# Performance work log

Hardware: AMD Instinct MI355X
Metric: run time of the kernel (lower is better)

## Reference

```python
import jax, jax.numpy as jnp
import numpy as np

N_NODES = 200_000
N_EDGES = 400_000
EMB_DIM = 128
HID_DIM = 24
N_TYPES = 8


def setup_inputs() -> dict:
    key = jax.random.key(0)
    k_emb, k_src, k_typ, k_w1, k_w2 = jax.random.split(key, 5)
    rgcn_emb = jax.random.normal(k_emb, (N_NODES, EMB_DIM), dtype=jnp.float32)
    edge_index = jax.random.randint(k_src, (2, N_EDGES), 0, N_NODES, dtype=jnp.int32)
    edge_type = jax.random.randint(k_typ, (N_EDGES,), 0, N_TYPES, dtype=jnp.int32)
    # per-edge-type 2-layer MLP params: Linear(2D->H), Linear(H->1)
    W1 = jax.random.normal(k_w1, (N_TYPES, 2 * EMB_DIM, HID_DIM), dtype=jnp.float32) * 0.05
    b1 = jnp.zeros((N_TYPES, HID_DIM), dtype=jnp.float32)
    W2 = jax.random.normal(k_w2, (N_TYPES, HID_DIM), dtype=jnp.float32) * 0.05
    b2 = jnp.zeros((N_TYPES,), dtype=jnp.float32)
    return {"rgcn_emb": rgcn_emb, "edge_index": edge_index, "edge_type": edge_type,
            "W1": W1, "b1": b1, "W2": W2, "b2": b2}


def reference(rgcn_emb, edge_index, edge_type, W1, b1, W2, b2):
    src, dst = edge_index[0], edge_index[1]
    # gather + concat: [E, 2D]
    edge_emb = jnp.concatenate([rgcn_emb[src], rgcn_emb[dst]], axis=-1)
    # dense per-type expert compute, then select by routing (MoE-style)
    h = jnp.einsum('ed,tdh->teh', edge_emb, W1) + b1[:, None, :]  # [T,E,H]
    h = jnp.where(h > 0, h, 0.01 * h)  # LeakyReLU(0.01)
    s = jnp.einsum('teh,th->te', h, W2) + b2[:, None]  # [T,E]
    onehot = jax.nn.one_hot(edge_type, N_TYPES, dtype=s.dtype)  # [E,T]
    scores = jnp.einsum('te,et->e', s, onehot)  # scatter-select per edge
    return (scores, rgcn_emb)
```

## Files before the change

kernel.cpp:

```cpp
#include <hip/hip_runtime.h>


typedef _Float16 h2 __attribute__((ext_vector_type(2)));

constexpr int N_NODES = 200000;
constexpr int N_EDGES = 400000;
constexpr int EMB_DIM = 128;
constexpr int HID     = 24;
constexpr int N_TYPES = 8;
constexpr int BLK     = 256;

constexpr int MAX_PAD      = N_EDGES + N_TYPES * (BLK - 1);
constexpr int SCORE_BLOCKS = (MAX_PAD + BLK - 1) / BLK;
constexpr int COPY_BLOCKS  = 1024;
constexpr int HIST_BLOCKS  = 128;
constexpr int SC_BLOCKS    = 128;
constexpr int SC_CH        = (N_EDGES + SC_BLOCKS - 1) / SC_BLOCKS;
constexpr int CV_BLOCKS    = 1536;

constexpr size_t SORT_BYTES = (size_t)(16 + MAX_PAD) * sizeof(int);
constexpr size_t EMB16_OFF  = (SORT_BYTES + 255) & ~(size_t)255;
constexpr size_t EMB16_BYTES = (size_t)N_NODES * EMB_DIM * 2;
constexpr size_t W16_OFF    = EMB16_OFF + EMB16_BYTES;
constexpr size_t W16_BYTES  = (size_t)N_TYPES * 128 * HID * 4;
constexpr size_t NEED16     = W16_OFF + W16_BYTES;

__device__ __forceinline__ float fdot2f(h2 a, h2 b, float c) {
#if __has_builtin(__builtin_amdgcn_fdot2)
    return __builtin_amdgcn_fdot2(a, b, c, false);
#else
    return c + (float)a[0] * (float)b[0] + (float)a[1] * (float)b[1];
#endif
}

__global__ __launch_bounds__(BLK) void hist_k(const int* __restrict__ etype,
                                              int* __restrict__ counts) {
    __shared__ int lc[N_TYPES];
    if (threadIdx.x < N_TYPES) lc[threadIdx.x] = 0;
    __syncthreads();
    for (int e = blockIdx.x * BLK + threadIdx.x; e < N_EDGES; e += HIST_BLOCKS * BLK)
        atomicAdd(&lc[etype[e]], 1);
    __syncthreads();
    if (threadIdx.x < N_TYPES) {
        int v = lc[threadIdx.x];
        if (v) atomicAdd(&counts[threadIdx.x], v);
    }
}

__global__ __launch_bounds__(BLK) void scatter_convert_k(
        const int* __restrict__ etype, int* __restrict__ counts,
        int* __restrict__ sorted,
        const float* __restrict__ emb, h2* __restrict__ emb16,
        const float* __restrict__ W1, h2* __restrict__ w16, int do16) {
    int b = blockIdx.x;
    if (b < SC_BLOCKS) {
        __shared__ int lc[N_TYPES], base[N_TYPES];
        if (threadIdx.x < N_TYPES) lc[threadIdx.x] = 0;
        __syncthreads();
        int e0 = b * SC_CH, e1 = min(e0 + SC_CH, N_EDGES);
        for (int e = e0 + threadIdx.x; e < e1; e += BLK)
            atomicAdd(&lc[etype[e]], 1);
        __syncthreads();
        if (threadIdx.x < N_TYPES)
            base[threadIdx.x] = atomicAdd(&counts[8 + threadIdx.x], lc[threadIdx.x]);
        __syncthreads();
        if (threadIdx.x < N_TYPES) lc[threadIdx.x] = 0;
        __syncthreads();
        int poff[N_TYPES];
        int off = 0;
#pragma unroll
        for (int t = 0; t < N_TYPES; ++t) {
            poff[t] = off;
            off += ((counts[t] + BLK - 1) / BLK) * BLK;
        }
        for (int e = e0 + threadIdx.x; e < e1; e += BLK) {
            int t = etype[e];
            int r = atomicAdd(&lc[t], 1);
            sorted[poff[t] + base[t] + r] = e;
        }
    } else if (do16) {
        int cb = b - SC_BLOCKS;
        if (cb < 16) {
            for (int p = cb * BLK + threadIdx.x; p < N_TYPES * 128 * HID; p += 16 * BLK) {
                int t   = p / (128 * HID);
                int rem = p - t * 128 * HID;
                int kp  = rem / HID, j = rem - kp * HID;
                h2 v;
                v[0] = (_Float16)W1[(t * 256 + 2 * kp)     * HID + j];
                v[1] = (_Float16)W1[(t * 256 + 2 * kp + 1) * HID + j];
                w16[p] = v;
            }
        }
        const float4* in4 = (const float4*)emb;
        int4* o16 = (int4*)emb16;
        const int ngrp = N_NODES * EMB_DIM / 8;
        for (int g = cb * BLK + threadIdx.x; g < ngrp; g += CV_BLOCKS * BLK) {
            float4 a = in4[2 * g], c = in4[2 * g + 1];
            union { int4 v; h2 h[4]; } u;
            u.h[0] = h2{(_Float16)a.x, (_Float16)a.y};
            u.h[1] = h2{(_Float16)a.z, (_Float16)a.w};
            u.h[2] = h2{(_Float16)c.x, (_Float16)c.y};
            u.h[3] = h2{(_Float16)c.z, (_Float16)c.w};
            o16[g] = u.v;
        }
    }
}

__device__ __forceinline__ void do_copy(const float* __restrict__ emb,
                                        float* __restrict__ out, int cb, int nb) {
    const float4* s4 = (const float4*)emb;
    float4* o4 = (float4*)(out + N_EDGES);
    const long long n4 = (long long)N_NODES * EMB_DIM / 4;
    long long stride = (long long)nb * BLK;
    for (long long i = (long long)cb * BLK + threadIdx.x; i < n4; i += stride)
        o4[i] = s4[i];
}

__global__ __launch_bounds__(BLK) void score16_k(
        const unsigned short* __restrict__ emb16u, const float* __restrict__ emb,
        const int* __restrict__ srci, const int* __restrict__ dsti,
        const int* __restrict__ counts, const int* __restrict__ sorted,
        const h2* __restrict__ w16, const float* __restrict__ b1,
        const float* __restrict__ W2, const float* __restrict__ b2,
        float* __restrict__ out) {
    int b = blockIdx.x;
    if (b >= SCORE_BLOCKS) {
        do_copy(emb, out, b - SCORE_BLOCKS, (int)gridDim.x - SCORE_BLOCKS);
        return;
    }
    int poff[N_TYPES];
    int off = 0;
#pragma unroll
    for (int t = 0; t < N_TYPES; ++t) {
        poff[t] = off;
        off += ((counts[t] + BLK - 1) / BLK) * BLK;
    }
    int slot0 = b * BLK;
    if (slot0 >= off) return;
    int t = 0;
#pragma unroll
    for (int i = 1; i < N_TYPES; ++i)
        if (slot0 >= poff[i]) t = i;
    t = __builtin_amdgcn_readfirstlane(t);
    int cnt = counts[t];
    int local = slot0 - poff[t] + (int)threadIdx.x;
    if (local >= cnt) return;
    int e = sorted[slot0 + threadIdx.x];
    int s = srci[e], d = dsti[e];

    float acc[HID];
#pragma unroll
    for (int j = 0; j < HID; ++j) acc[j] = b1[t * HID + j];
    const h2* wt = w16 + (size_t)t * 128 * HID;
    const int4* x0 = (const int4*)(emb16u + (size_t)s * EMB_DIM);
    const int4* x1 = (const int4*)(emb16u + (size_t)d * EMB_DIM);

#pragma unroll 1
    for (int half = 0; half < 2; ++half) {
        const int4* xp = half ? x1 : x0;
#pragma unroll 1
        for (int c = 0; c < 2; ++c) {
            int4 r[8];
#pragma unroll
            for (int k = 0; k < 8; ++k) r[k] = xp[c * 8 + k];
            const h2* hp = (const h2*)r;
            const h2* wrow = wt + (half * 64 + c * 32) * HID;
#pragma unroll
            for (int kp = 0; kp < 32; ++kp) {
#pragma unroll
                for (int j = 0; j < HID; ++j)
                    acc[j] = fdot2f(hp[kp], wrow[kp * HID + j], acc[j]);
            }
        }
    }
    float sc = b2[t];
#pragma unroll
    for (int j = 0; j < HID; ++j) {
        float h = acc[j];
        h = (h > 0.f) ? h : 0.01f * h;
        sc = fmaf(h, W2[t * HID + j], sc);
    }
    out[e] = sc;
}

__device__ __forceinline__ void half_mm(const float4* __restrict__ x4,
                                        const float* __restrict__ w,
                                        float acc[HID]) {
#pragma unroll 1
    for (int c = 0; c < 4; ++c) {
        float4 r[8];
#pragma unroll
        for (int k = 0; k < 8; ++k) r[k] = x4[c * 8 + k];
#pragma unroll
        for (int k = 0; k < 8; ++k) {
            const float* wp = w + (c * 32 + k * 4) * HID;
#pragma unroll
            for (int j = 0; j < HID; ++j) acc[j] = fmaf(r[k].x, wp[0 * HID + j], acc[j]);
#pragma unroll
            for (int j = 0; j < HID; ++j) acc[j] = fmaf(r[k].y, wp[1 * HID + j], acc[j]);
#pragma unroll
            for (int j = 0; j < HID; ++j) acc[j] = fmaf(r[k].z, wp[2 * HID + j], acc[j]);
#pragma unroll
            for (int j = 0; j < HID; ++j) acc[j] = fmaf(r[k].w, wp[3 * HID + j], acc[j]);
        }
    }
}

__global__ __launch_bounds__(BLK) void score32_k(
        const float* __restrict__ emb,
        const int* __restrict__ srci, const int* __restrict__ dsti,
        const int* __restrict__ counts, const int* __restrict__ sorted,
        const float* __restrict__ W1, const float* __restrict__ b1,
        const float* __restrict__ W2, const float* __restrict__ b2,
        float* __restrict__ out) {
    int b = blockIdx.x;
    if (b >= SCORE_BLOCKS) {
        do_copy(emb, out, b - SCORE_BLOCKS, (int)gridDim.x - SCORE_BLOCKS);
        return;
    }
    int poff[N_TYPES];
    int off = 0;
#pragma unroll
    for (int t = 0; t < N_TYPES; ++t) {
        poff[t] = off;
        off += ((counts[t] + BLK - 1) / BLK) * BLK;
    }
    int slot0 = b * BLK;
    if (slot0 >= off) return;
    int t = 0;
#pragma unroll
    for (int i = 1; i < N_TYPES; ++i)
        if (slot0 >= poff[i]) t = i;
    t = __builtin_amdgcn_readfirstlane(t);
    int cnt = counts[t];
    int local = slot0 - poff[t] + (int)threadIdx.x;
    if (local >= cnt) return;
    int e = sorted[slot0 + threadIdx.x];
    float acc[HID];
#pragma unroll
    for (int j = 0; j < HID; ++j) acc[j] = b1[t * HID + j];
    const float* W1t = W1 + (size_t)t * (2 * EMB_DIM * HID);
    int s = srci[e], d = dsti[e];
    half_mm((const float4*)(emb + (size_t)s * EMB_DIM), W1t, acc);
    half_mm((const float4*)(emb + (size_t)d * EMB_DIM), W1t + EMB_DIM * HID, acc);
    float sc = b2[t];
#pragma unroll
    for (int j = 0; j < HID; ++j) {
        float h = acc[j];
        h = (h > 0.f) ? h : 0.01f * h;
        sc = fmaf(h, W2[t * HID + j], sc);
    }
    out[e] = sc;
}

extern "C" void kernel_launch(void* const* d_in, const int* in_sizes, int n_in,
                              void* d_out, int out_size, void* d_ws, size_t ws_size,
                              hipStream_t stream) {
    const float* emb   = (const float*)d_in[0];
    const int*   eidx  = (const int*)d_in[1];
    const int*   etype = (const int*)d_in[2];
    const float* W1    = (const float*)d_in[3];
    const float* b1    = (const float*)d_in[4];
    const float* W2    = (const float*)d_in[5];
    const float* b2    = (const float*)d_in[6];
    float* out = (float*)d_out;
    const int* srci = eidx;
    const int* dsti = eidx + N_EDGES;

    if (ws_size >= SORT_BYTES) {
        int* counts = (int*)d_ws;
        int* sorted = counts + 16;
        bool f16 = (ws_size >= NEED16);
        h2* emb16 = (h2*)((char*)d_ws + EMB16_OFF);
        h2* w16   = (h2*)((char*)d_ws + W16_OFF);
        hipMemsetAsync(counts, 0, 16 * sizeof(int), stream);
        hist_k<<<HIST_BLOCKS, BLK, 0, stream>>>(etype, counts);
        scatter_convert_k<<<SC_BLOCKS + (f16 ? CV_BLOCKS : 0), BLK, 0, stream>>>(
            etype, counts, sorted, emb, emb16, W1, w16, f16 ? 1 : 0);
        if (f16) {
            score16_k<<<SCORE_BLOCKS + COPY_BLOCKS, BLK, 0, stream>>>(
                (const unsigned short*)emb16, emb, srci, dsti, counts, sorted,
                w16, b1, W2, b2, out);
        } else {
            score32_k<<<SCORE_BLOCKS + COPY_BLOCKS, BLK, 0, stream>>>(
                emb, srci, dsti, counts, sorted, W1, b1, W2, b2, out);
        }
    } else {
        score32_k<<<SCORE_BLOCKS + COPY_BLOCKS, BLK, 0, stream>>>(
            emb, srci, dsti, nullptr, nullptr, W1, b1, W2, b2, out);
    }
}
```

Baseline: 278.1 us.

## Fuse embedding copy into fp16 conversion pass and double-buffer row loads

The pass-through copy of rgcn_emb to the output moves into the prep kernel, so each fp32 element is read once, with nontemporal loads and stores, and both copied and converted to fp16. The histogram folds into the same prep launch using int4 loads of edge types, and the scatter becomes its own kernel. The score kernel no longer carries copy blocks and issues the next 128-byte chunk load before computing the current one, to overlap gather latency with the dot products. The fallback path becomes a simple unsorted fp32 kernel.

```diff
diff --git a/kernel.cpp b/kernel.cpp
--- a/kernel.cpp
+++ b/kernel.cpp
@@ -2,6 +2,7 @@
 
 
 typedef _Float16 h2 __attribute__((ext_vector_type(2)));
+typedef float    f4 __attribute__((ext_vector_type(4)));
 
 constexpr int N_NODES = 200000;
 constexpr int N_EDGES = 400000;
@@ -12,18 +13,20 @@
 
 constexpr int MAX_PAD      = N_EDGES + N_TYPES * (BLK - 1);
 constexpr int SCORE_BLOCKS = (MAX_PAD + BLK - 1) / BLK;
-constexpr int COPY_BLOCKS  = 1024;
-constexpr int HIST_BLOCKS  = 128;
 constexpr int SC_BLOCKS    = 128;
 constexpr int SC_CH        = (N_EDGES + SC_BLOCKS - 1) / SC_BLOCKS;
-constexpr int CV_BLOCKS    = 1536;
-
-constexpr size_t SORT_BYTES = (size_t)(16 + MAX_PAD) * sizeof(int);
-constexpr size_t EMB16_OFF  = (SORT_BYTES + 255) & ~(size_t)255;
+
+constexpr int PREP_HIST   = 64;
+constexpr int PREP_W1     = 16;
+constexpr int PREP_CONV   = 1968;
+constexpr int PREP_BLOCKS = PREP_HIST + PREP_W1 + PREP_CONV;
+
+constexpr size_t SORT_BYTES  = (size_t)(16 + MAX_PAD) * sizeof(int);
+constexpr size_t EMB16_OFF   = (SORT_BYTES + 255) & ~(size_t)255;
 constexpr size_t EMB16_BYTES = (size_t)N_NODES * EMB_DIM * 2;
-constexpr size_t W16_OFF    = EMB16_OFF + EMB16_BYTES;
-constexpr size_t W16_BYTES  = (size_t)N_TYPES * 128 * HID * 4;
-constexpr size_t NEED16     = W16_OFF + W16_BYTES;
+constexpr size_t W16_OFF     = EMB16_OFF + EMB16_BYTES;
+constexpr size_t W16_BYTES   = (size_t)N_TYPES * 128 * HID * 4;
+constexpr size_t NEED16      = W16_OFF + W16_BYTES;
 
 __device__ __forceinline__ float fdot2f(h2 a, h2 b, float c) {
 #if __has_builtin(__builtin_amdgcn_fdot2)
@@ -33,101 +36,103 @@
 #endif
 }
 
-__global__ __launch_bounds__(BLK) void hist_k(const int* __restrict__ etype,
-                                              int* __restrict__ counts) {
-    __shared__ int lc[N_TYPES];
-    if (threadIdx.x < N_TYPES) lc[threadIdx.x] = 0;
-    __syncthreads();
-    for (int e = blockIdx.x * BLK + threadIdx.x; e < N_EDGES; e += HIST_BLOCKS * BLK)
-        atomicAdd(&lc[etype[e]], 1);
-    __syncthreads();
-    if (threadIdx.x < N_TYPES) {
-        int v = lc[threadIdx.x];
-        if (v) atomicAdd(&counts[threadIdx.x], v);
-    }
-}
-
-__global__ __launch_bounds__(BLK) void scatter_convert_k(
+__global__ __launch_bounds__(BLK) void prep_k(
         const int* __restrict__ etype, int* __restrict__ counts,
-        int* __restrict__ sorted,
-        const float* __restrict__ emb, h2* __restrict__ emb16,
-        const float* __restrict__ W1, h2* __restrict__ w16, int do16) {
+        const float* __restrict__ emb, float* __restrict__ out,
+        int2* __restrict__ emb16, const float* __restrict__ W1,
+        h2* __restrict__ w16) {
     int b = blockIdx.x;
-    if (b < SC_BLOCKS) {
-        __shared__ int lc[N_TYPES], base[N_TYPES];
+    if (b < PREP_HIST) {
+        __shared__ int lc[N_TYPES];
         if (threadIdx.x < N_TYPES) lc[threadIdx.x] = 0;
         __syncthreads();
-        int e0 = b * SC_CH, e1 = min(e0 + SC_CH, N_EDGES);
-        for (int e = e0 + threadIdx.x; e < e1; e += BLK)
-            atomicAdd(&lc[etype[e]], 1);
+        const int4* et4 = (const int4*)etype;
+        for (int g = b * BLK + threadIdx.x; g < N_EDGES / 4; g += PREP_HIST * BLK) {
+            int4 v = et4[g];
+            atomicAdd(&lc[v.x], 1); atomicAdd(&lc[v.y], 1);
+            atomicAdd(&lc[v.z], 1); atomicAdd(&lc[v.w], 1);
+        }
         __syncthreads();
-        if (threadIdx.x < N_TYPES)
-            base[threadIdx.x] = atomicAdd(&counts[8 + threadIdx.x], lc[threadIdx.x]);
-        __syncthreads();
-        if (threadIdx.x < N_TYPES) lc[threadIdx.x] = 0;
-        __syncthreads();
-        int poff[N_TYPES];
-        int off = 0;
-#pragma unroll
-        for (int t = 0; t < N_TYPES; ++t) {
-            poff[t] = off;
-            off += ((counts[t] + BLK - 1) / BLK) * BLK;
-        }
-        for (int e = e0 + threadIdx.x; e < e1; e += BLK) {
-            int t = etype[e];
-            int r = atomicAdd(&lc[t], 1);
-            sorted[poff[t] + base[t] + r] = e;
-        }
-    } else if (do16) {
-        int cb = b - SC_BLOCKS;
-        if (cb < 16) {
-            for (int p = cb * BLK + threadIdx.x; p < N_TYPES * 128 * HID; p += 16 * BLK) {
-                int t   = p / (128 * HID);
-                int rem = p - t * 128 * HID;
-                int kp  = rem / HID, j = rem - kp * HID;
-                h2 v;
-                v[0] = (_Float16)W1[(t * 256 + 2 * kp)     * HID + j];
-                v[1] = (_Float16)W1[(t * 256 + 2 * kp + 1) * HID + j];
-                w16[p] = v;
-            }
-        }
-        const float4* in4 = (const float4*)emb;
-        int4* o16 = (int4*)emb16;
-        const int ngrp = N_NODES * EMB_DIM / 8;
-        for (int g = cb * BLK + threadIdx.x; g < ngrp; g += CV_BLOCKS * BLK) {
-            float4 a = in4[2 * g], c = in4[2 * g + 1];
-            union { int4 v; h2 h[4]; } u;
+        if (threadIdx.x < N_TYPES) {
+            int v = lc[threadIdx.x];
+            if (v) atomicAdd(&counts[threadIdx.x], v);
+        }
+    } else if (b < PREP_HIST + PREP_W1) {
+        int cb = b - PREP_HIST;
+        for (int p = cb * BLK + threadIdx.x; p < N_TYPES * 128 * HID; p += PREP_W1 * BLK) {
+            int t   = p / (128 * HID);
+            int rem = p - t * 128 * HID;
+            int kp  = rem / HID, j = rem - kp * HID;
+            h2 v;
+            v[0] = (_Float16)W1[(t * 256 + 2 * kp)     * HID + j];
+            v[1] = (_Float16)W1[(t * 256 + 2 * kp + 1) * HID + j];
+            w16[p] = v;
+        }
+    } else {
+        int cb = b - PREP_HIST - PREP_W1;
+        const f4* in4 = (const f4*)emb;
+        f4* o4 = (f4*)(out + N_EDGES);
+        const int n4 = N_NODES * EMB_DIM / 4;
+        for (int i = cb * BLK + threadIdx.x; i < n4; i += PREP_CONV * BLK) {
+            f4 a = __builtin_nontemporal_load(&in4[i]);
+            __builtin_nontemporal_store(a, &o4[i]);
+            union { int2 v; h2 h[2]; } u;
             u.h[0] = h2{(_Float16)a.x, (_Float16)a.y};
             u.h[1] = h2{(_Float16)a.z, (_Float16)a.w};
-            u.h[2] = h2{(_Float16)c.x, (_Float16)c.y};
-            u.h[3] = h2{(_Float16)c.z, (_Float16)c.w};
-            o16[g] = u.v;
-        }
-    }
-}
-
-__device__ __forceinline__ void do_copy(const float* __restrict__ emb,
-                                        float* __restrict__ out, int cb, int nb) {
-    const float4* s4 = (const float4*)emb;
-    float4* o4 = (float4*)(out + N_EDGES);
-    const long long n4 = (long long)N_NODES * EMB_DIM / 4;
-    long long stride = (long long)nb * BLK;
-    for (long long i = (long long)cb * BLK + threadIdx.x; i < n4; i += stride)
-        o4[i] = s4[i];
-}
-
-__global__ __launch_bounds__(BLK) void score16_k(
-        const unsigned short* __restrict__ emb16u, const float* __restrict__ emb,
+            emb16[i] = u.v;
+        }
+    }
+}
+
+__global__ __launch_bounds__(BLK) void scatter_k(
+        const int* __restrict__ etype, int* __restrict__ counts,
+        int* __restrict__ sorted) {
+    __shared__ int lc[N_TYPES], base[N_TYPES];
+    int b = blockIdx.x;
+    if (threadIdx.x < N_TYPES) lc[threadIdx.x] = 0;
+    __syncthreads();
+    int e0 = b * SC_CH, e1 = min(e0 + SC_CH, N_EDGES);
+    for (int e = e0 + threadIdx.x; e < e1; e += BLK)
+        atomicAdd(&lc[etype[e]], 1);
+    __syncthreads();
+    if (threadIdx.x < N_TYPES)
+        base[threadIdx.x] = atomicAdd(&counts[8 + threadIdx.x], lc[threadIdx.x]);
+    __syncthreads();
+    if (threadIdx.x < N_TYPES) lc[threadIdx.x] = 0;
+    __syncthreads();
+    int poff[N_TYPES];
+    int off = 0;
+#pragma unroll
+    for (int t = 0; t < N_TYPES; ++t) {
+        poff[t] = off;
+        off += ((counts[t] + BLK - 1) / BLK) * BLK;
+    }
+    for (int e = e0 + threadIdx.x; e < e1; e += BLK) {
+        int t = etype[e];
+        int r = atomicAdd(&lc[t], 1);
+        sorted[poff[t] + base[t] + r] = e;
+    }
+}
+
+__device__ __forceinline__ void compute_chunk(const int4* __restrict__ r,
+                                              const h2* __restrict__ wrow,
+                                              float acc[HID]) {
+    const h2* hp = (const h2*)r;
+#pragma unroll
+    for (int kp = 0; kp < 32; ++kp) {
+#pragma unroll
+        for (int j = 0; j < HID; ++j)
+            acc[j] = fdot2f(hp[kp], wrow[kp * HID + j], acc[j]);
+    }
+}
+
+__global__ __launch_bounds__(BLK) void score16_ns_k(
+        const unsigned short* __restrict__ emb16u,
         const int* __restrict__ srci, const int* __restrict__ dsti,
         const int* __restrict__ counts, const int* __restrict__ sorted,
         const h2* __restrict__ w16, const float* __restrict__ b1,
         const float* __restrict__ W2, const float* __restrict__ b2,
         float* __restrict__ out) {
-    int b = blockIdx.x;
-    if (b >= SCORE_BLOCKS) {
-        do_copy(emb, out, b - SCORE_BLOCKS, (int)gridDim.x - SCORE_BLOCKS);
-        return;
-    }
     int poff[N_TYPES];
     int off = 0;
 #pragma unroll
@@ -135,7 +140,7 @@
         poff[t] = off;
         off += ((counts[t] + BLK - 1) / BLK) * BLK;
     }
-    int slot0 = b * BLK;
+    int slot0 = blockIdx.x * BLK;
     if (slot0 >= off) return;
     int t = 0;
 #pragma unroll
@@ -155,24 +160,20 @@
     const int4* x0 = (const int4*)(emb16u + (size_t)s * EMB_DIM);
     const int4* x1 = (const int4*)(emb16u + (size_t)d * EMB_DIM);
 
-#pragma unroll 1
-    for (int half = 0; half < 2; ++half) {
-        const int4* xp = half ? x1 : x0;
-#pragma unroll 1
-        for (int c = 0; c < 2; ++c) {
-            int4 r[8];
-#pragma unroll
-            for (int k = 0; k < 8; ++k) r[k] = xp[c * 8 + k];
-            const h2* hp = (const h2*)r;
-            const h2* wrow = wt + (half * 64 + c * 32) * HID;
-#pragma unroll
-            for (int kp = 0; kp < 32; ++kp) {
-#pragma unroll
-                for (int j = 0; j < HID; ++j)
-                    acc[j] = fdot2f(hp[kp], wrow[kp * HID + j], acc[j]);
-            }
-        }
-    }
+    int4 A[8], B[8];
+#pragma unroll
+    for (int k = 0; k < 8; ++k) A[k] = x0[k];
+#pragma unroll
+    for (int k = 0; k < 8; ++k) B[k] = x0[8 + k];
+    compute_chunk(A, wt + 0 * 32 * HID, acc);
+#pragma unroll
+    for (int k = 0; k < 8; ++k) A[k] = x1[k];
+    compute_chunk(B, wt + 1 * 32 * HID, acc);
+#pragma unroll
+    for (int k = 0; k < 8; ++k) B[k] = x1[8 + k];
+    compute_chunk(A, wt + 2 * 32 * HID, acc);
+    compute_chunk(B, wt + 3 * 32 * HID, acc);
+
     float sc = b2[t];
 #pragma unroll
     for (int j = 0; j < HID; ++j) {
@@ -183,74 +184,45 @@
     out[e] = sc;
 }
 
-__device__ __forceinline__ void half_mm(const float4* __restrict__ x4,
-                                        const float* __restrict__ w,
-                                        float acc[HID]) {
-#pragma unroll 1
-    for (int c = 0; c < 4; ++c) {
-        float4 r[8];
-#pragma unroll
-        for (int k = 0; k < 8; ++k) r[k] = x4[c * 8 + k];
-#pragma unroll
-        for (int k = 0; k < 8; ++k) {
-            const float* wp = w + (c * 32 + k * 4) * HID;
-#pragma unroll
-            for (int j = 0; j < HID; ++j) acc[j] = fmaf(r[k].x, wp[0 * HID + j], acc[j]);
-#pragma unroll
-            for (int j = 0; j < HID; ++j) acc[j] = fmaf(r[k].y, wp[1 * HID + j], acc[j]);
-#pragma unroll
-            for (int j = 0; j < HID; ++j) acc[j] = fmaf(r[k].z, wp[2 * HID + j], acc[j]);
-#pragma unroll
-            for (int j = 0; j < HID; ++j) acc[j] = fmaf(r[k].w, wp[3 * HID + j], acc[j]);
-        }
-    }
-}
-
-__global__ __launch_bounds__(BLK) void score32_k(
+__global__ __launch_bounds__(BLK) void fallback_k(
         const float* __restrict__ emb,
         const int* __restrict__ srci, const int* __restrict__ dsti,
-        const int* __restrict__ counts, const int* __restrict__ sorted,
+        const int* __restrict__ etype,
         const float* __restrict__ W1, const float* __restrict__ b1,
         const float* __restrict__ W2, const float* __restrict__ b2,
         float* __restrict__ out) {
-    int b = blockIdx.x;
-    if (b >= SCORE_BLOCKS) {
-        do_copy(emb, out, b - SCORE_BLOCKS, (int)gridDim.x - SCORE_BLOCKS);
-        return;
-    }
-    int poff[N_TYPES];
-    int off = 0;
-#pragma unroll
-    for (int t = 0; t < N_TYPES; ++t) {
-        poff[t] = off;
-        off += ((counts[t] + BLK - 1) / BLK) * BLK;
-    }
-    int slot0 = b * BLK;
-    if (slot0 >= off) return;
-    int t = 0;
-#pragma unroll
-    for (int i = 1; i < N_TYPES; ++i)
-        if (slot0 >= poff[i]) t = i;
-    t = __builtin_amdgcn_readfirstlane(t);
-    int cnt = counts[t];
-    int local = slot0 - poff[t] + (int)threadIdx.x;
-    if (local >= cnt) return;
-    int e = sorted[slot0 + threadIdx.x];
-    float acc[HID];
-#pragma unroll
-    for (int j = 0; j < HID; ++j) acc[j] = b1[t * HID + j];
-    const float* W1t = W1 + (size_t)t * (2 * EMB_DIM * HID);
-    int s = srci[e], d = dsti[e];
-    half_mm((const float4*)(emb + (size_t)s * EMB_DIM), W1t, acc);
-    half_mm((const float4*)(emb + (size_t)d * EMB_DIM), W1t + EMB_DIM * HID, acc);
-    float sc = b2[t];
-#pragma unroll
-    for (int j = 0; j < HID; ++j) {
-        float h = acc[j];
-        h = (h > 0.f) ? h : 0.01f * h;
-        sc = fmaf(h, W2[t * HID + j], sc);
-    }
-    out[e] = sc;
+    long long i0 = (long long)blockIdx.x * BLK + threadIdx.x;
+    const float4* s4 = (const float4*)emb;
+    float4* o4 = (float4*)(out + N_EDGES);
+    const long long n4 = (long long)N_NODES * EMB_DIM / 4;
+    for (long long i = i0; i < n4; i += (long long)gridDim.x * BLK)
+        o4[i] = s4[i];
+    for (int e = (int)i0; e < N_EDGES; e += gridDim.x * BLK) {
+        int t = etype[e];
+        int s = srci[e], d = dsti[e];
+        float acc[HID];
+#pragma unroll
+        for (int j = 0; j < HID; ++j) acc[j] = b1[t * HID + j];
+        const float* w = W1 + (size_t)t * 2 * EMB_DIM * HID;
+        for (int k = 0; k < EMB_DIM; ++k) {
+            float x = emb[(size_t)s * EMB_DIM + k];
+#pragma unroll
+            for (int j = 0; j < HID; ++j) acc[j] = fmaf(x, w[k * HID + j], acc[j]);
+        }
+        for (int k = 0; k < EMB_DIM; ++k) {
+            float x = emb[(size_t)d * EMB_DIM + k];
+#pragma unroll
+            for (int j = 0; j < HID; ++j) acc[j] = fmaf(x, w[(EMB_DIM + k) * HID + j], acc[j]);
+        }
+        float sc = b2[t];
+#pragma unroll
+        for (int j = 0; j < HID; ++j) {
+            float h = acc[j];
+            h = (h > 0.f) ? h : 0.01f * h;
+            sc = fmaf(h, W2[t * HID + j], sc);
+        }
+        out[e] = sc;
+    }
 }
 
 extern "C" void kernel_launch(void* const* d_in, const int* in_sizes, int n_in,
@@ -267,26 +239,18 @@
     const int* srci = eidx;
     const int* dsti = eidx + N_EDGES;
 
-    if (ws_size >= SORT_BYTES) {
+    if (ws_size >= NEED16) {
         int* counts = (int*)d_ws;
         int* sorted = counts + 16;
-        bool f16 = (ws_size >= NEED16);
-        h2* emb16 = (h2*)((char*)d_ws + EMB16_OFF);
-        h2* w16   = (h2*)((char*)d_ws + W16_OFF);
-        hipMemsetAsync(counts, 0, 16 * sizeof(int), stream);
-        hist_k<<<HIST_BLOCKS, BLK, 0, stream>>>(etype, counts);
-        scatter_convert_k<<<SC_BLOCKS + (f16 ? CV_BLOCKS : 0), BLK, 0, stream>>>(
-            etype, counts, sorted, emb, emb16, W1, w16, f16 ? 1 : 0);
-        if (f16) {
-            score16_k<<<SCORE_BLOCKS + COPY_BLOCKS, BLK, 0, stream>>>(
-                (const unsigned short*)emb16, emb, srci, dsti, counts, sorted,
-                w16, b1, W2, b2, out);
-        } else {
-            score32_k<<<SCORE_BLOCKS + COPY_BLOCKS, BLK, 0, stream>>>(
-                emb, srci, dsti, counts, sorted, W1, b1, W2, b2, out);
-        }
+        int2* emb16 = (int2*)((char*)d_ws + EMB16_OFF);
+        h2*   w16   = (h2*)((char*)d_ws + W16_OFF);
+        (void)hipMemsetAsync(counts, 0, 16 * sizeof(int), stream);
+        prep_k<<<PREP_BLOCKS, BLK, 0, stream>>>(etype, counts, emb, out, emb16, W1, w16);
+        scatter_k<<<SC_BLOCKS, BLK, 0, stream>>>(etype, counts, sorted);
+        score16_ns_k<<<SCORE_BLOCKS, BLK, 0, stream>>>(
+            (const unsigned short*)emb16, srci, dsti, counts, sorted,
+            w16, b1, W2, b2, out);
     } else {
-        score32_k<<<SCORE_BLOCKS + COPY_BLOCKS, BLK, 0, stream>>>(
-            emb, srci, dsti, nullptr, nullptr, W1, b1, W2, b2, out);
-    }
-}
+        fallback_k<<<2048, BLK, 0, stream>>>(emb, srci, dsti, etype, W1, b1, W2, b2, out);
+    }
+}
```

Result: slower. 287.0 us (+3.2%).
